# Kernel tuning notes

Measured on AMD Instinct MI355X. Metric: run time of the kernel, lower is better.

The kernel has to match this reference:

```python
import jax, jax.numpy as jnp
import numpy as np

EPS = 1e-10


def setup_inputs() -> dict:
    key = jax.random.key(0)
    k1, k2 = jax.random.split(key)
    B, N = 4096, 10000
    pred = jax.random.uniform(k1, (B, N), dtype=jnp.float32)
    y = jax.random.randint(k2, (B, N), 0, 2, dtype=jnp.int32)
    return {"pred": pred, "y": y, "lamda": 5}


def reference(pred, y, lamda):
    # per-element weighted BCE-style term:
    #   y==0 -> -log(1 - p + eps); y!=0 -> -lamda * log(p + eps)
    neg_term = -jnp.log1p(-(pred - EPS))          # -log(1 - p + eps)
    pos_term = -lamda * jnp.log(pred + EPS)
    elem = jnp.where(y == 0, neg_term, pos_term)  # [B, N]
    # mean over elements per sample, then mean over batch; keep shape (1,) like torch.zeros(1)
    loss = jnp.mean(elem)
    return loss.reshape(1)
```

## Files before the change

### kernel.cpp

```cpp
#include <hip/hip_runtime.h>
#include <hip/hip_bf16.h>

#define EPS 1e-10f
#define BLOCK 256
#define GRID1 2048
#define TILE_VEC (BLOCK * 8)


__global__ __launch_bounds__(BLOCK) void sparse_loss_stage1(
    const float* __restrict__ pred,
    const int* __restrict__ y,
    const int* __restrict__ lamda_p,
    float* __restrict__ partials,
    long long nvec,
    long long total) {
  const float lam = (float)(*lamda_p);
  float acc = 0.0f;

  const float4* __restrict__ pv = reinterpret_cast<const float4*>(pred);
  const int4* __restrict__ yv = reinterpret_cast<const int4*>(y);

  const long long ntiles = (nvec + TILE_VEC - 1) / TILE_VEC;
  const int tid = threadIdx.x;

#define ELEM(P, Y)                                              \
  {                                                             \
    const bool z = ((Y) == 0);                                  \
    const float a = EPS + (z ? (1.0f - (P)) : (P));             \
    const float c = z ? 1.0f : lam;                             \
    acc = fmaf(c, __logf(a), acc);                              \
  }

  for (long long tile = blockIdx.x; tile < ntiles; tile += gridDim.x) {
    const long long base = tile * TILE_VEC;
    const float4* __restrict__ pt = pv + base;
    const int4* __restrict__ yt = yv + base;
    const long long rem = nvec - base;

    if (rem >= TILE_VEC) {
      float4 p[8];
      int4 yy[8];
#pragma unroll
      for (int k = 0; k < 8; ++k) p[k] = pt[tid + BLOCK * k];
#pragma unroll
      for (int k = 0; k < 8; ++k) yy[k] = yt[tid + BLOCK * k];
#pragma unroll
      for (int k = 0; k < 8; ++k) {
        ELEM(p[k].x, yy[k].x)
        ELEM(p[k].y, yy[k].y)
        ELEM(p[k].z, yy[k].z)
        ELEM(p[k].w, yy[k].w)
      }
    } else {
      for (long long j = tid; j < rem; j += BLOCK) {
        const float4 p = pt[j];
        const int4 yy = yt[j];
        ELEM(p.x, yy.x)
        ELEM(p.y, yy.y)
        ELEM(p.z, yy.z)
        ELEM(p.w, yy.w)
      }
    }
  }

  const long long gtid = (long long)blockIdx.x * BLOCK + tid;
  const long long gstride = (long long)gridDim.x * BLOCK;
  for (long long j = nvec * 4 + gtid; j < total; j += gstride) {
    const float p = pred[j];
    ELEM(p, y[j])
  }
#undef ELEM

  for (int off = 32; off > 0; off >>= 1)
    acc += __shfl_down(acc, off, 64);

  __shared__ float ssum[4];
  const int lane = tid & 63;
  const int wave = tid >> 6;
  if (lane == 0) ssum[wave] = acc;
  __syncthreads();

  if (tid == 0)
    partials[blockIdx.x] = ssum[0] + ssum[1] + ssum[2] + ssum[3];
}

__global__ __launch_bounds__(BLOCK) void sparse_loss_stage2(
    const float* __restrict__ partials,
    float* __restrict__ out,
    float inv_total) {
  float acc = 0.0f;
  for (int i = threadIdx.x; i < GRID1; i += BLOCK)
    acc += partials[i];

  for (int off = 32; off > 0; off >>= 1)
    acc += __shfl_down(acc, off, 64);

  __shared__ float ssum[4];
  const int lane = threadIdx.x & 63;
  const int wave = threadIdx.x >> 6;
  if (lane == 0) ssum[wave] = acc;
  __syncthreads();

  if (threadIdx.x == 0)
    out[0] = -(ssum[0] + ssum[1] + ssum[2] + ssum[3]) * inv_total;
}

extern "C" void kernel_launch(void* const* d_in, const int* in_sizes, int n_in,
                              void* d_out, int out_size, void* d_ws, size_t ws_size,
                              hipStream_t stream) {
  const float* pred = (const float*)d_in[0];
  const int* y = (const int*)d_in[1];
  const int* lamda = (const int*)d_in[2];
  float* out = (float*)d_out;
  float* partials = (float*)d_ws;

  const long long total = (long long)in_sizes[0];
  const long long nvec = total / 4;
  const float inv_total = 1.0f / (float)total;

  sparse_loss_stage1<<<GRID1, BLOCK, 0, stream>>>(pred, y, lamda, partials,
                                                  nvec, total);
  sparse_loss_stage2<<<1, BLOCK, 0, stream>>>(partials, out, inv_total);
}
```

Baseline: 330.1 us.

## Stream inputs through per-wave double-buffered LDS via global_load_lds

Replaces the register-tiled float4 grid-stride loop with a per-wave pipeline. Each wave gets a contiguous range of 1 KB steps and prefetches the next step of pred and y into a double-buffered LDS slot with global_load_lds, using manual s_waitcnt to overlap the copy with compute. It also switches to log2 and applies ln2 once in the final reduction, saving a multiply per element. In exchange, each wave keeps only one 16-byte load per array in flight, which lowers memory-level parallelism compared with the 16 outstanding loads per thread before.

Result: slower. 339.4 us (+2.8%).

```diff
diff --git a/kernel.cpp b/kernel.cpp
--- a/kernel.cpp
+++ b/kernel.cpp
@@ -1,11 +1,20 @@
 #include <hip/hip_runtime.h>
 #include <hip/hip_bf16.h>
+#include <stdint.h>
 
 #define EPS 1e-10f
 #define BLOCK 256
 #define GRID1 2048
-#define TILE_VEC (BLOCK * 8)
+#define WPB 4
+#define STEP_BYTES 1024
+#define LN2F 0.69314718055994530942f
 
+
+__device__ __forceinline__ void glds16(const void* g, void* l) {
+  __builtin_amdgcn_global_load_lds(
+      (const __attribute__((address_space(1))) unsigned int*)g,
+      (__attribute__((address_space(3))) unsigned int*)l, 16, 0, 0);
+}
 
 __global__ __launch_bounds__(BLOCK) void sparse_loss_stage1(
     const float* __restrict__ pred,
@@ -14,58 +23,71 @@
     float* __restrict__ partials,
     long long nvec,
     long long total) {
+  __shared__ __align__(16) unsigned char lds[WPB][2][2 * STEP_BYTES];
+  __shared__ float ssum[WPB];
+
+  const int tid = threadIdx.x;
+  const int wave = tid >> 6;
+  const int lane = tid & 63;
   const float lam = (float)(*lamda_p);
   float acc = 0.0f;
-
-  const float4* __restrict__ pv = reinterpret_cast<const float4*>(pred);
-  const int4* __restrict__ yv = reinterpret_cast<const int4*>(y);
-
-  const long long ntiles = (nvec + TILE_VEC - 1) / TILE_VEC;
-  const int tid = threadIdx.x;
 
 #define ELEM(P, Y)                                              \
   {                                                             \
     const bool z = ((Y) == 0);                                  \
     const float a = EPS + (z ? (1.0f - (P)) : (P));             \
-    const float c = z ? 1.0f : lam;                             \
-    acc = fmaf(c, __logf(a), acc);                              \
+    acc = fmaf(z ? 1.0f : lam, __log2f(a), acc);                \
   }
 
-  for (long long tile = blockIdx.x; tile < ntiles; tile += gridDim.x) {
-    const long long base = tile * TILE_VEC;
-    const float4* __restrict__ pt = pv + base;
-    const int4* __restrict__ yt = yv + base;
-    const long long rem = nvec - base;
+  const long long nsteps = nvec >> 6;
+  const long long wid = (long long)blockIdx.x * WPB + wave;
+  const long long nw = (long long)gridDim.x * WPB;
+  const long long s0 = (wid * nsteps) / nw;
+  const long long s1 = ((wid + 1) * nsteps) / nw;
 
-    if (rem >= TILE_VEC) {
-      float4 p[8];
-      int4 yy[8];
-#pragma unroll
-      for (int k = 0; k < 8; ++k) p[k] = pt[tid + BLOCK * k];
-#pragma unroll
-      for (int k = 0; k < 8; ++k) yy[k] = yt[tid + BLOCK * k];
-#pragma unroll
-      for (int k = 0; k < 8; ++k) {
-        ELEM(p[k].x, yy[k].x)
-        ELEM(p[k].y, yy[k].y)
-        ELEM(p[k].z, yy[k].z)
-        ELEM(p[k].w, yy[k].w)
-      }
+  const char* pb = (const char*)pred;
+  const char* yb = (const char*)y;
+  char* const lp0 = (char*)&lds[wave][0][0];
+  char* const lp1 = (char*)&lds[wave][1][0];
+
+#define STAGE(S, LB)                                                       \
+  {                                                                        \
+    asm volatile("s_waitcnt lgkmcnt(0)" ::: "memory");                     \
+    const long long off_ = (S) * (long long)STEP_BYTES + lane * 16;        \
+    glds16(pb + off_, (LB));                                               \
+    glds16(yb + off_, (LB) + STEP_BYTES);                                  \
+  }
+
+  if (s0 < s1) STAGE(s0, lp0);
+  for (long long s = s0; s < s1; ++s) {
+    char* const lb = ((s - s0) & 1) ? lp1 : lp0;
+    if (s + 1 < s1) {
+      char* const nb = ((s - s0) & 1) ? lp0 : lp1;
+      STAGE(s + 1, nb);
+      asm volatile("s_waitcnt vmcnt(2)" ::: "memory");
     } else {
-      for (long long j = tid; j < rem; j += BLOCK) {
-        const float4 p = pt[j];
-        const int4 yy = yt[j];
-        ELEM(p.x, yy.x)
-        ELEM(p.y, yy.y)
-        ELEM(p.z, yy.z)
-        ELEM(p.w, yy.w)
-      }
+      asm volatile("s_waitcnt vmcnt(0)" ::: "memory");
     }
+    const float4 p = *(const float4*)(lb + lane * 16);
+    const int4 yy = *(const int4*)(lb + STEP_BYTES + lane * 16);
+    ELEM(p.x, yy.x)
+    ELEM(p.y, yy.y)
+    ELEM(p.z, yy.z)
+    ELEM(p.w, yy.w)
   }
+#undef STAGE
 
   const long long gtid = (long long)blockIdx.x * BLOCK + tid;
   const long long gstride = (long long)gridDim.x * BLOCK;
-  for (long long j = nvec * 4 + gtid; j < total; j += gstride) {
+  for (long long j = (nsteps << 6) + gtid; j < nvec; j += gstride) {
+    const float4 p = reinterpret_cast<const float4*>(pred)[j];
+    const int4 yy = reinterpret_cast<const int4*>(y)[j];
+    ELEM(p.x, yy.x)
+    ELEM(p.y, yy.y)
+    ELEM(p.z, yy.z)
+    ELEM(p.w, yy.w)
+  }
+  for (long long j = (nvec << 2) + gtid; j < total; j += gstride) {
     const float p = pred[j];
     ELEM(p, y[j])
   }
@@ -74,9 +96,6 @@
   for (int off = 32; off > 0; off >>= 1)
     acc += __shfl_down(acc, off, 64);
 
-  __shared__ float ssum[4];
-  const int lane = tid & 63;
-  const int wave = tid >> 6;
   if (lane == 0) ssum[wave] = acc;
   __syncthreads();
 
@@ -101,8 +120,9 @@
   if (lane == 0) ssum[wave] = acc;
   __syncthreads();
 
-  if (threadIdx.x == 0)
-    out[0] = -(ssum[0] + ssum[1] + ssum[2] + ssum[3]) * inv_total;
+  if (threadIdx.x == 0) {
+    out[0] = -(ssum[0] + ssum[1] + ssum[2] + ssum[3]) * inv_total * LN2F;
+  }
 }
 
 extern "C" void kernel_launch(void* const* d_in, const int* in_sizes, int n_in,
```
